# Performance work log

Measured on AMD Instinct MI355X. Metric: run time of the kernel, lower is better.

The kernel has to match this reference:

```python
import jax, jax.numpy as jnp
import numpy as np

DIM = 1024
HIDDEN = 3072
SCALE = 1.0 / 127.0  # fixed Q8_0-style dequant scale from QuantizedLinear


def setup_inputs() -> dict:
    key = jax.random.key(0)
    k_x, k_g, k_u, k_d = jax.random.split(key, 4)
    x = jax.random.normal(k_x, (4, 2048, DIM), dtype=jnp.float32)
    # int8-valued quantized weights stored as int32 (symmetric range like torch int8 weights)
    w_gate = jax.random.randint(k_g, (HIDDEN, DIM), -127, 128, dtype=jnp.int32)
    w_up = jax.random.randint(k_u, (HIDDEN, DIM), -127, 128, dtype=jnp.int32)
    w_down = jax.random.randint(k_d, (DIM, HIDDEN), -127, 128, dtype=jnp.int32)
    return {"x": x, "w_gate": w_gate, "w_up": w_up, "w_down": w_down}


def _dequant(w_int, dtype):
    return w_int.astype(dtype) * jnp.asarray(SCALE, dtype)


def reference(x, w_gate, w_up, w_down):
    # QuantizedLinear: dequantize int8 weight to x.dtype, then F.linear (x @ W^T)
    wg = _dequant(w_gate, x.dtype)   # [H, D]
    wu = _dequant(w_up, x.dtype)     # [H, D]
    wd = _dequant(w_down, x.dtype)   # [D, H]
    gate = jnp.einsum('bsd,hd->bsh', x, wg)
    up = jnp.einsum('bsd,hd->bsh', x, wu)
    h = jax.nn.silu(gate) * up       # SwiGLU elementwise fusion
    return jnp.einsum('bsh,dh->bsd', h, wd)
```

## Files before the change

### kernel.cpp

```cpp
#include <hip/hip_runtime.h>
#include <hip/hip_bf16.h>


typedef __attribute__((ext_vector_type(8))) __bf16 bf16x8;
typedef __attribute__((ext_vector_type(4))) float f32x4;

static constexpr float QS = 1.0f / 127.0f;

__device__ __forceinline__ void gload_lds16(const void* g, void* l) {
  __builtin_amdgcn_global_load_lds(
      (const __attribute__((address_space(1))) void*)g,
      (__attribute__((address_space(3))) void*)l,
      16, 0, 0);
}


__global__ __launch_bounds__(256) void k_conv_x(const float* __restrict__ x,
                                                __bf16* __restrict__ xb, int n8) {
  int t = blockIdx.x * 256 + threadIdx.x;
  if (t >= n8) return;
  const float4* p = (const float4*)(x + (size_t)t * 8);
  float4 a = p[0], b = p[1];
  bf16x8 o;
  o[0] = (__bf16)a.x; o[1] = (__bf16)a.y; o[2] = (__bf16)a.z; o[3] = (__bf16)a.w;
  o[4] = (__bf16)b.x; o[5] = (__bf16)b.y; o[6] = (__bf16)b.z; o[7] = (__bf16)b.w;
  *(bf16x8*)(xb + (size_t)t * 8) = o;
}

__global__ __launch_bounds__(256) void k_conv_w1(const int* __restrict__ wg,
                                                 const int* __restrict__ wu,
                                                 __bf16* __restrict__ w1) {
  int t = blockIdx.x * 256 + threadIdx.x;
  int c8 = t & 127;
  int v = t >> 7;
  int bb = v >> 5, tt = v & 31;
  const int* src = (tt < 16) ? (wg + (size_t)(bb * 16 + tt) * 1024)
                             : (wu + (size_t)(bb * 16 + (tt & 15)) * 1024);
  const int4* p = (const int4*)(src + c8 * 8);
  int4 a = p[0], b = p[1];
  bf16x8 o;
  o[0] = (__bf16)(float)a.x; o[1] = (__bf16)(float)a.y;
  o[2] = (__bf16)(float)a.z; o[3] = (__bf16)(float)a.w;
  o[4] = (__bf16)(float)b.x; o[5] = (__bf16)(float)b.y;
  o[6] = (__bf16)(float)b.z; o[7] = (__bf16)(float)b.w;
  *(bf16x8*)(w1 + (size_t)v * 1024 + c8 * 8) = o;
}

__global__ __launch_bounds__(256) void k_conv_wd(const int* __restrict__ wdn,
                                                 __bf16* __restrict__ wdb, int n8) {
  int t = blockIdx.x * 256 + threadIdx.x;
  if (t >= n8) return;
  const int4* p = (const int4*)(wdn + (size_t)t * 8);
  int4 a = p[0], b = p[1];
  bf16x8 o;
  o[0] = (__bf16)(float)a.x; o[1] = (__bf16)(float)a.y;
  o[2] = (__bf16)(float)a.z; o[3] = (__bf16)(float)a.w;
  o[4] = (__bf16)(float)b.x; o[5] = (__bf16)(float)b.y;
  o[6] = (__bf16)(float)b.z; o[7] = (__bf16)(float)b.w;
  *(bf16x8*)(wdb + (size_t)t * 8) = o;
}

template <int MODE>
__device__ __forceinline__ void gemm_body(const __bf16* __restrict__ A,
                                          const __bf16* __restrict__ B,
                                          void* __restrict__ Out,
                                          int lda, int nkt, int ldo,
                                          int row0, int col0, int kz) {
  __shared__ __bf16 sA[128][64];
  __shared__ __bf16 sB[128][64];
  const int tid = threadIdx.x;
  const int lane = tid & 63;
  const int wid = tid >> 6;
  const int wm = wid >> 1, wn = wid & 1;
  const int r16 = lane & 15;
  const int kq = lane >> 4;

  f32x4 acc[4][4] = {};

  for (int kt = kz; kt < kz + nkt; ++kt) {
    __syncthreads();
#pragma unroll
    for (int it = 0; it < 4; ++it) {
      int chunk = it * 256 + tid;
      int r = chunk >> 3, kc = chunk & 7;
      int kcs = kc ^ (r & 7);
      gload_lds16(A + (size_t)(row0 + r) * lda + kt * 64 + kcs * 8,
                  ((__bf16*)sA) + chunk * 8);
      gload_lds16(B + (size_t)(col0 + r) * lda + kt * 64 + kcs * 8,
                  ((__bf16*)sB) + chunk * 8);
    }
    __syncthreads();
#pragma unroll
    for (int ks = 0; ks < 2; ++ks) {
      const int chs = ((ks * 4 + kq) ^ (r16 & 7)) << 4;
      bf16x8 av[4], bv[4];
#pragma unroll
      for (int i = 0; i < 4; ++i)
        av[i] = *(const bf16x8*)(((const char*)sA) +
                                 (wm * 64 + i * 16 + r16) * 128 + chs);
#pragma unroll
      for (int j = 0; j < 4; ++j)
        bv[j] = *(const bf16x8*)(((const char*)sB) +
                                 (wn * 64 + j * 16 + r16) * 128 + chs);
#pragma unroll
      for (int i = 0; i < 4; ++i)
#pragma unroll
        for (int j = 0; j < 4; ++j)
          acc[i][j] = __builtin_amdgcn_mfma_f32_16x16x32_bf16(av[i], bv[j],
                                                              acc[i][j], 0, 0, 0);
    }
  }

  if constexpr (MODE == 1) {
    __bf16* hout = (__bf16*)Out;
    const int hbase = (col0 + wn * 64) >> 1;
#pragma unroll
    for (int i = 0; i < 4; ++i) {
#pragma unroll
      for (int p = 0; p < 2; ++p) {
#pragma unroll
        for (int r = 0; r < 4; ++r) {
          int row = row0 + wm * 64 + i * 16 + kq * 4 + r;
          float g = acc[i][2 * p][r] * QS;
          float u = acc[i][2 * p + 1][r] * QS;
          float hv = (g / (1.0f + __expf(-g))) * u;
          hout[(size_t)row * ldo + hbase + p * 16 + r16] = (__bf16)hv;
        }
      }
    }
  } else {
    float* out = (float*)Out;
#pragma unroll
    for (int i = 0; i < 4; ++i)
#pragma unroll
      for (int j = 0; j < 4; ++j)
#pragma unroll
        for (int r = 0; r < 4; ++r) {
          int row = row0 + wm * 64 + i * 16 + kq * 4 + r;
          int col = col0 + wn * 64 + j * 16 + r16;
          out[(size_t)row * ldo + col] = acc[i][j][r] * QS;
        }
  }
}

__global__ __launch_bounds__(256) void k_gemm1(const __bf16* __restrict__ A,
                                               const __bf16* __restrict__ B,
                                               __bf16* __restrict__ H) {
  gemm_body<1>(A, B, H, 1024, 16, 3072, blockIdx.y * 128, blockIdx.x * 128, 0);
}

__global__ __launch_bounds__(256) void k_gemm2(const __bf16* __restrict__ H,
                                               const __bf16* __restrict__ B,
                                               float* __restrict__ P) {
  int b = blockIdx.x;
  int w = (b & 7) * 128 + (b >> 3);
  int z = w >> 9;
  int rem = w & 511;
  int y = rem >> 3, x = rem & 7;
  gemm_body<0>(H, B, P + (size_t)z * (8192 * 1024), 3072, 24, 1024,
               y * 128, x * 128, z * 24);
}

__global__ __launch_bounds__(256) void k_reduce2(const float* __restrict__ p,
                                                 float* __restrict__ out, int n4) {
  int t = blockIdx.x * 256 + threadIdx.x;
  if (t >= n4) return;
  const float4* a = (const float4*)p;
  const float4* b = (const float4*)(p + (size_t)8192 * 1024);
  float4 va = a[t], vb = b[t];
  ((float4*)out)[t] = make_float4(va.x + vb.x, va.y + vb.y,
                                  va.z + vb.z, va.w + vb.w);
}

__global__ __launch_bounds__(256) void k_gemm2_nosplit(const __bf16* __restrict__ H,
                                                       const __bf16* __restrict__ B,
                                                       float* __restrict__ O) {
  gemm_body<0>(H, B, O, 3072, 48, 1024, blockIdx.y * 128, blockIdx.x * 128, 0);
}


extern "C" void kernel_launch(void* const* d_in, const int* in_sizes, int n_in,
                              void* d_out, int out_size, void* d_ws, size_t ws_size,
                              hipStream_t stream) {
  const float* x = (const float*)d_in[0];
  const int* wg = (const int*)d_in[1];
  const int* wu = (const int*)d_in[2];
  const int* wd = (const int*)d_in[3];

  char* ws = (char*)d_ws;
  __bf16* xb  = (__bf16*)(ws);
  __bf16* w1  = (__bf16*)(ws + 16777216);
  __bf16* wdb = (__bf16*)(ws + 16777216 + 12582912);
  __bf16* h   = (__bf16*)(ws + 35651584);
  float*  part = (float*)(ws + 85983232);
  const bool splitk = ws_size >= (size_t)85983232 + 2u * 33554432u;

  k_conv_x<<<4096, 256, 0, stream>>>(x, xb, 1048576);
  k_conv_w1<<<3072, 256, 0, stream>>>(wg, wu, w1);
  k_conv_wd<<<1536, 256, 0, stream>>>(wd, wdb, 393216);

  k_gemm1<<<dim3(48, 64), 256, 0, stream>>>(xb, w1, h);

  if (splitk) {
    k_gemm2<<<1024, 256, 0, stream>>>(h, wdb, part);
    k_reduce2<<<8192, 256, 0, stream>>>(part, (float*)d_out, 2097152);
  } else {
    k_gemm2_nosplit<<<dim3(8, 64), 256, 0, stream>>>(h, wdb, (float*)d_out);
  }
}
```

Baseline: 314.1 us.

## Rewrite GEMMs as 256x256 8-wave tiles with double-buffered LDS pipeline

Replaces the 128x128, 4-wave GEMM body with a 256x256 tile run by 8 waves (512 threads) over a double-buffered LDS ring of half-tiles. Global-to-LDS loads for the next K steps are interleaved between MFMA groups, using explicit s_barrier and vmcnt waits plus s_setprio to raise MFMA priority. The aim is to raise arithmetic intensity per byte loaded and hide load latency behind compute. In exchange it uses 128KB of LDS and far more accumulator registers, and the tile remapping leaves fewer blocks for gemm2, which risks lower occupancy and tail imbalance.

```diff
diff --git a/kernel.cpp b/kernel.cpp
--- a/kernel.cpp
+++ b/kernel.cpp
@@ -6,6 +6,12 @@
 typedef __attribute__((ext_vector_type(4))) float f32x4;
 
 static constexpr float QS = 1.0f / 127.0f;
+
+#define BAR()   asm volatile("s_barrier" ::: "memory")
+#define VMCNT4() asm volatile("s_waitcnt vmcnt(4)" ::: "memory")
+#define VMCNT0() asm volatile("s_waitcnt vmcnt(0)" ::: "memory")
+#define PRIO1() __builtin_amdgcn_s_setprio(1)
+#define PRIO0() __builtin_amdgcn_s_setprio(0)
 
 __device__ __forceinline__ void gload_lds16(const void* g, void* l) {
   __builtin_amdgcn_global_load_lds(
@@ -60,105 +66,154 @@
   *(bf16x8*)(wdb + (size_t)t * 8) = o;
 }
 
-template <int MODE>
-__device__ __forceinline__ void gemm_body(const __bf16* __restrict__ A,
-                                          const __bf16* __restrict__ B,
-                                          void* __restrict__ Out,
-                                          int lda, int nkt, int ldo,
-                                          int row0, int col0, int kz) {
-  __shared__ __bf16 sA[128][64];
-  __shared__ __bf16 sB[128][64];
+
+#define MFMA16(MG, NG)                                                         \
+  _Pragma("unroll") for (int mi = 0; mi < 4; ++mi) {                           \
+    _Pragma("unroll") for (int nj = 0; nj < 2; ++nj) {                         \
+      acc[(MG)*4 + mi][(NG)*2 + nj] = __builtin_amdgcn_mfma_f32_16x16x32_bf16( \
+          af[mi][0], bf[NG][nj][0], acc[(MG)*4 + mi][(NG)*2 + nj], 0, 0, 0);   \
+      acc[(MG)*4 + mi][(NG)*2 + nj] = __builtin_amdgcn_mfma_f32_16x16x32_bf16( \
+          af[mi][1], bf[NG][nj][1], acc[(MG)*4 + mi][(NG)*2 + nj], 0, 0, 0);   \
+    }                                                                          \
+  }
+
+#define LDAF(MG)                                                               \
+  _Pragma("unroll") for (int mi = 0; mi < 4; ++mi) {                           \
+    af[mi][0] = *(const bf16x8*)(aL + ((MG)*64 + mi * 16 + r16) * 128 + s0);   \
+    af[mi][1] = *(const bf16x8*)(aL + ((MG)*64 + mi * 16 + r16) * 128 + s1);   \
+  }
+
+#define LDBF(NG)                                                               \
+  _Pragma("unroll") for (int nj = 0; nj < 2; ++nj) {                           \
+    bf[NG][nj][0] = *(const bf16x8*)(bL + (bro + (NG)*32 + nj * 16) * 128 + s0); \
+    bf[NG][nj][1] = *(const bf16x8*)(bL + (bro + (NG)*32 + nj * 16) * 128 + s1); \
+  }
+
+template <int MODE, int LDAK, int NT, int LDO>
+__device__ __forceinline__ void gemm8_body(const __bf16* __restrict__ A,
+                                           const __bf16* __restrict__ Bp,
+                                           void* __restrict__ Out,
+                                           int row0, int col0, int kz) {
+  __shared__ __bf16 sA[2][2][128][64];
+  __shared__ __bf16 sB[2][2][128][64];
   const int tid = threadIdx.x;
   const int lane = tid & 63;
   const int wid = tid >> 6;
-  const int wm = wid >> 1, wn = wid & 1;
+  const int wm = wid >> 2, wn = wid & 3;
   const int r16 = lane & 15;
   const int kq = lane >> 4;
 
-  f32x4 acc[4][4] = {};
-
-  for (int kt = kz; kt < kz + nkt; ++kt) {
-    __syncthreads();
-#pragma unroll
-    for (int it = 0; it < 4; ++it) {
-      int chunk = it * 256 + tid;
-      int r = chunk >> 3, kc = chunk & 7;
-      int kcs = kc ^ (r & 7);
-      gload_lds16(A + (size_t)(row0 + r) * lda + kt * 64 + kcs * 8,
-                  ((__bf16*)sA) + chunk * 8);
-      gload_lds16(B + (size_t)(col0 + r) * lda + kt * 64 + kcs * 8,
-                  ((__bf16*)sB) + chunk * 8);
-    }
-    __syncthreads();
-#pragma unroll
-    for (int ks = 0; ks < 2; ++ks) {
-      const int chs = ((ks * 4 + kq) ^ (r16 & 7)) << 4;
-      bf16x8 av[4], bv[4];
-#pragma unroll
-      for (int i = 0; i < 4; ++i)
-        av[i] = *(const bf16x8*)(((const char*)sA) +
-                                 (wm * 64 + i * 16 + r16) * 128 + chs);
-#pragma unroll
-      for (int j = 0; j < 4; ++j)
-        bv[j] = *(const bf16x8*)(((const char*)sB) +
-                                 (wn * 64 + j * 16 + r16) * 128 + chs);
-#pragma unroll
-      for (int i = 0; i < 4; ++i)
-#pragma unroll
-        for (int j = 0; j < 4; ++j)
-          acc[i][j] = __builtin_amdgcn_mfma_f32_16x16x32_bf16(av[i], bv[j],
-                                                              acc[i][j], 0, 0, 0);
-    }
+  auto STG = [&](__bf16* dst, const __bf16* src, int rbase, int kt) {
+    int r0 = tid >> 3;
+    int c0 = (tid & 7) ^ (r0 & 7);
+    int r1 = 64 + r0;
+    gload_lds16(src + (size_t)(rbase + r0) * LDAK + kt * 64 + c0 * 8,
+                dst + tid * 8);
+    gload_lds16(src + (size_t)(rbase + r1) * LDAK + kt * 64 + c0 * 8,
+                dst + (512 + tid) * 8);
+  };
+
+  f32x4 acc[8][4] = {};
+
+  STG(&sA[0][0][0][0], A, row0, kz);
+  STG(&sB[0][0][0][0], Bp, col0, kz);
+  STG(&sA[0][1][0][0], A, row0 + 128, kz);
+  STG(&sB[0][1][0][0], Bp, col0 + 128, kz);
+  const int kt1 = kz + (NT > 1 ? 1 : 0);
+  STG(&sB[1][0][0][0], Bp, col0, kt1);
+  STG(&sA[1][0][0][0], A, row0, kt1);
+  VMCNT4();
+  BAR();
+
+  for (int t = 0; t < NT; ++t) {
+    const int c = t & 1;
+    const char* aL = (const char*)&sA[c][wm][0][0];
+    const char* bL = (const char*)&sB[c][wn >> 1][0][0];
+    const int bro = (wn & 1) * 64 + r16;
+    const int s0 = ((kq) ^ (r16 & 7)) << 4;
+    const int s1 = ((4 + kq) ^ (r16 & 7)) << 4;
+    const int k1 = kz + (t + 1 < NT ? t + 1 : NT - 1);
+    const int k2 = kz + (t + 2 < NT ? t + 2 : NT - 1);
+    bf16x8 af[4][2], bf[2][2][2];
+
+    LDAF(0);
+    LDBF(0);
+    STG(&sA[c ^ 1][1][0][0], A, row0 + 128, k1);
+    BAR();
+    PRIO1(); MFMA16(0, 0); PRIO0();
+    BAR();
+    LDBF(1);
+    STG(&sB[c ^ 1][1][0][0], Bp, col0 + 128, k1);
+    BAR();
+    PRIO1(); MFMA16(0, 1); PRIO0();
+    BAR();
+    LDAF(1);
+    STG(&sB[c][0][0][0], Bp, col0, k2);
+    BAR();
+    PRIO1(); MFMA16(1, 0); PRIO0();
+    BAR();
+    STG(&sA[c][0][0][0], A, row0, k2);
+    BAR();
+    PRIO1(); MFMA16(1, 1); PRIO0();
+    VMCNT4();
+    BAR();
   }
 
   if constexpr (MODE == 1) {
     __bf16* hout = (__bf16*)Out;
     const int hbase = (col0 + wn * 64) >> 1;
 #pragma unroll
-    for (int i = 0; i < 4; ++i) {
+    for (int i = 0; i < 8; ++i) {
 #pragma unroll
       for (int p = 0; p < 2; ++p) {
 #pragma unroll
-        for (int r = 0; r < 4; ++r) {
-          int row = row0 + wm * 64 + i * 16 + kq * 4 + r;
-          float g = acc[i][2 * p][r] * QS;
-          float u = acc[i][2 * p + 1][r] * QS;
+        for (int rr = 0; rr < 4; ++rr) {
+          int row = row0 + wm * 128 + i * 16 + kq * 4 + rr;
+          float g = acc[i][2 * p][rr] * QS;
+          float u = acc[i][2 * p + 1][rr] * QS;
           float hv = (g / (1.0f + __expf(-g))) * u;
-          hout[(size_t)row * ldo + hbase + p * 16 + r16] = (__bf16)hv;
+          hout[(size_t)row * LDO + hbase + p * 16 + r16] = (__bf16)hv;
         }
       }
     }
   } else {
     float* out = (float*)Out;
 #pragma unroll
-    for (int i = 0; i < 4; ++i)
+    for (int i = 0; i < 8; ++i)
 #pragma unroll
       for (int j = 0; j < 4; ++j)
 #pragma unroll
-        for (int r = 0; r < 4; ++r) {
-          int row = row0 + wm * 64 + i * 16 + kq * 4 + r;
+        for (int rr = 0; rr < 4; ++rr) {
+          int row = row0 + wm * 128 + i * 16 + kq * 4 + rr;
           int col = col0 + wn * 64 + j * 16 + r16;
-          out[(size_t)row * ldo + col] = acc[i][j][r] * QS;
+          out[(size_t)row * LDO + col] = acc[i][j][rr] * QS;
         }
   }
-}
-
-__global__ __launch_bounds__(256) void k_gemm1(const __bf16* __restrict__ A,
-                                               const __bf16* __restrict__ B,
-                                               __bf16* __restrict__ H) {
-  gemm_body<1>(A, B, H, 1024, 16, 3072, blockIdx.y * 128, blockIdx.x * 128, 0);
-}
-
-__global__ __launch_bounds__(256) void k_gemm2(const __bf16* __restrict__ H,
-                                               const __bf16* __restrict__ B,
-                                               float* __restrict__ P) {
+  VMCNT0();
+}
+
+__global__ __launch_bounds__(512, 2) void k_gemm1_8p(const __bf16* __restrict__ A,
+                                                     const __bf16* __restrict__ B,
+                                                     __bf16* __restrict__ H) {
+  gemm8_body<1, 1024, 16, 3072>(A, B, H, blockIdx.y * 256, blockIdx.x * 256, 0);
+}
+
+__global__ __launch_bounds__(512, 2) void k_gemm2_8p(const __bf16* __restrict__ H,
+                                                     const __bf16* __restrict__ B,
+                                                     float* __restrict__ P) {
   int b = blockIdx.x;
-  int w = (b & 7) * 128 + (b >> 3);
-  int z = w >> 9;
-  int rem = w & 511;
-  int y = rem >> 3, x = rem & 7;
-  gemm_body<0>(H, B, P + (size_t)z * (8192 * 1024), 3072, 24, 1024,
-               y * 128, x * 128, z * 24);
+  int w = (b & 7) * 32 + (b >> 3);
+  int z = w >> 7;
+  int rem = w & 127;
+  int y = rem >> 2, x = rem & 3;
+  gemm8_body<0, 3072, 24, 1024>(H, B, P + (size_t)z * (8192 * 1024),
+                                y * 256, x * 256, z * 24);
+}
+
+__global__ __launch_bounds__(512, 2) void k_gemm2_8p_ns(const __bf16* __restrict__ H,
+                                                        const __bf16* __restrict__ B,
+                                                        float* __restrict__ O) {
+  gemm8_body<0, 3072, 48, 1024>(H, B, O, blockIdx.y * 256, blockIdx.x * 256, 0);
 }
 
 __global__ __launch_bounds__(256) void k_reduce2(const float* __restrict__ p,
@@ -170,12 +225,6 @@
   float4 va = a[t], vb = b[t];
   ((float4*)out)[t] = make_float4(va.x + vb.x, va.y + vb.y,
                                   va.z + vb.z, va.w + vb.w);
-}
-
-__global__ __launch_bounds__(256) void k_gemm2_nosplit(const __bf16* __restrict__ H,
-                                                       const __bf16* __restrict__ B,
-                                                       float* __restrict__ O) {
-  gemm_body<0>(H, B, O, 3072, 48, 1024, blockIdx.y * 128, blockIdx.x * 128, 0);
 }
 
 
@@ -199,12 +248,12 @@
   k_conv_w1<<<3072, 256, 0, stream>>>(wg, wu, w1);
   k_conv_wd<<<1536, 256, 0, stream>>>(wd, wdb, 393216);
 
-  k_gemm1<<<dim3(48, 64), 256, 0, stream>>>(xb, w1, h);
+  k_gemm1_8p<<<dim3(24, 32), 512, 0, stream>>>(xb, w1, h);
 
   if (splitk) {
-    k_gemm2<<<1024, 256, 0, stream>>>(h, wdb, part);
+    k_gemm2_8p<<<256, 512, 0, stream>>>(h, wdb, part);
     k_reduce2<<<8192, 256, 0, stream>>>(part, (float*)d_out, 2097152);
   } else {
-    k_gemm2_nosplit<<<dim3(8, 64), 256, 0, stream>>>(h, wdb, (float*)d_out);
-  }
-}
+    k_gemm2_8p_ns<<<dim3(4, 32), 512, 0, stream>>>(h, wdb, (float*)d_out);
+  }
+}
```

Result: faster. 298.5 us (-5.0%).
